# Kernel optimization log

Measured on AMD Instinct MI355X. Metric: run time of the kernel, lower is better.

## Reference

```python
import jax, jax.numpy as jnp
import numpy as np

N, E = 50000, 800000
F_IN, C1, H1 = 128, 16, 4        # conv1: 128 -> 16 per head, 4 heads (concat -> 64)
F_MID = C1 * H1                   # 64
N_CLASSES, H2 = 10, 1             # conv2: 64 -> 10, 1 head, no concat
NEG_SLOPE = 0.2


def setup_inputs() -> dict:
    key = jax.random.key(0)
    ks = jax.random.split(key, 12)
    s1 = 1.0 / np.sqrt(F_IN)
    s2 = 1.0 / np.sqrt(F_MID)
    return {
        "x": jax.random.normal(ks[0], (N, F_IN), dtype=jnp.float32),
        "edge_index": jax.random.randint(ks[1], (2, E), 0, N, dtype=jnp.int64),
        # conv1 params (GATv2: separate lin_l / lin_r, per-head attention vector, bias)
        "W1l": jax.random.normal(ks[2], (F_IN, H1 * C1), dtype=jnp.float32) * s1,
        "W1r": jax.random.normal(ks[3], (F_IN, H1 * C1), dtype=jnp.float32) * s1,
        "att1": jax.random.normal(ks[4], (H1, C1), dtype=jnp.float32) * s1,
        "b1": jnp.zeros((H1 * C1,), dtype=jnp.float32),
        # conv2 params
        "W2l": jax.random.normal(ks[5], (F_MID, H2 * N_CLASSES), dtype=jnp.float32) * s2,
        "W2r": jax.random.normal(ks[6], (F_MID, H2 * N_CLASSES), dtype=jnp.float32) * s2,
        "att2": jax.random.normal(ks[7], (H2, N_CLASSES), dtype=jnp.float32) * s2,
        "b2": jnp.zeros((N_CLASSES,), dtype=jnp.float32),
    }


def gatv2_conv(x, Wl, Wr, att, b, src, dst, concat):
    """GATv2Conv (add_self_loops=False, eval mode). src -> dst message passing."""
    H, C = att.shape
    n = x.shape[0]
    xl = (x @ Wl).reshape(n, H, C)   # source-side transform (also the value)
    xr = (x @ Wr).reshape(n, H, C)   # target-side transform
    # per-edge GATv2 score: att . LeakyReLU(xl[src] + xr[dst])
    e = jax.nn.leaky_relu(xl[src] + xr[dst], NEG_SLOPE)          # [E, H, C]
    logits = jnp.einsum("ehc,hc->eh", e, att)                    # [E, H]
    # segment softmax over incoming edges of each dst node
    m = jax.ops.segment_max(logits, dst, num_segments=n)         # [N, H]
    ex = jnp.exp(logits - m[dst])
    denom = jax.ops.segment_sum(ex, dst, num_segments=n)         # [N, H]
    alpha = ex / denom[dst]                                      # [E, H]
    out = jax.ops.segment_sum(alpha[:, :, None] * xl[src], dst, num_segments=n)  # [N, H, C]
    out = out.reshape(n, H * C) if concat else out.mean(axis=1)
    return out + b


def reference(x, edge_index, W1l, W1r, att1, b1, W2l, W2r, att2, b2):
    src, dst = edge_index[0], edge_index[1]
    h = jax.nn.elu(gatv2_conv(x, W1l, W1r, att1, b1, src, dst, concat=True))
    return gatv2_conv(h, W2l, W2r, att2, b2, src, dst, concat=False)
```

## Files before the change

kernel.cpp:

```cpp
#include <hip/hip_runtime.h>
#include <math.h>

#define NN 50000
#define NE 800000
#define FIN 128
#define NC 10
#define NEG 0.2f

#define NB 196
#define CHUNK 4096
#define P1B ((NE + CHUNK - 1) / CHUNK)
#define CAP 5120
#define G1T ((NN + 127) / 128)

typedef unsigned int uint;
typedef unsigned char uchar;
typedef _Float16 h2 __attribute__((ext_vector_type(2)));
typedef __fp16 hb2 __attribute__((ext_vector_type(2)));
union U2H { uint u; h2 h; };

__device__ __forceinline__ uint pkrtz_u(float a, float b) {
    union { hb2 f; uint u; } r;
    r.f = __builtin_amdgcn_cvt_pkrtz(a, b);
    return r.u;
}

__device__ __forceinline__ float dot2f(h2 a, h2 b, float c) {
#if __has_builtin(__builtin_amdgcn_fdot2)
    return __builtin_amdgcn_fdot2(a, b, c, false);
#else
    return fmaf((float)a.x, (float)b.x, fmaf((float)a.y, (float)b.y, c));
#endif
}

__device__ __forceinline__ h2 lrelu2(h2 v) {
    return __builtin_elementwise_max(v, v * (_Float16)0.2f);
}

template<int CTRL>
__device__ __forceinline__ float dpp_add(float x) {
    int y = __builtin_amdgcn_update_dpp(0, __float_as_int(x), CTRL, 0xF, 0xF, true);
    return x + __int_as_float(y);
}
__device__ __forceinline__ float red8(float t) {
    t = dpp_add<0xB1>(t);
    t = dpp_add<0x4E>(t);
    t = dpp_add<0x141>(t);
    return t;
}

__device__ __forceinline__ int excl_scan256(int v, int* sc) {
    const int t = threadIdx.x;
    sc[t] = v;
    __syncthreads();
    for (int o = 1; o < 256; o <<= 1) {
        int u = (t >= o) ? sc[t - o] : 0;
        __syncthreads();
        sc[t] += u;
        __syncthreads();
    }
    return sc[t] - v;
}


__global__ void k_zinit(int* __restrict__ g) {
    if (threadIdx.x < NB) g[threadIdx.x] = 0;
}


__device__ void pass1_body(const int* __restrict__ ei, uint* __restrict__ temp,
                           int* __restrict__ gcursor, char* smraw) {
    uint*  pk = (uint*)smraw;
    uchar* bk = (uchar*)(smraw + 16384);
    int* h  = (int*)(smraw + 20480);
    int* h2_ = (int*)(smraw + 21504);
    int* gb = (int*)(smraw + 22528);
    int* lb = (int*)(smraw + 23552);
    int* sc = (int*)(smraw + 24576);
    const int t = threadIdx.x;
    const int e0 = blockIdx.x * CHUNK;
    const int cnt = min(CHUNK, NE - e0);

    h[t] = 0; h2_[t] = 0;
    __syncthreads();
    for (int i = t; i < cnt; i += 256) {
        int d = ei[NE + e0 + i];
        atomicAdd(&h[d >> 8], 1);
    }
    __syncthreads();
    const int hv = h[t];
    const int ex = excl_scan256(hv, sc);
    lb[t] = ex;
    if (t < NB && hv > 0) gb[t] = atomicAdd(&gcursor[t], hv);
    __syncthreads();
    for (int i = t; i < cnt; i += 256) {
        int s = ei[e0 + i];
        int d = ei[NE + e0 + i];
        int b = d >> 8;
        int r = atomicAdd(&h2_[b], 1);
        int pos = lb[b] + r;
        pk[pos] = ((uint)s << 8) | ((uint)d & 255u);
        bk[pos] = (uchar)b;
    }
    __syncthreads();
    for (int i = t; i < cnt; i += 256) {
        uint v = pk[i];
        int b = bk[i];
        int pos = gb[b] + (i - lb[b]);
        if (pos < CAP) temp[b * CAP + pos] = v;
    }
}

__device__ void gemm1_body(const float* __restrict__ x, const float* __restrict__ W,
                           uint* __restrict__ oh2, int n0, char* smraw) {
    uint (*Wsh)[64]  = (uint(*)[64])smraw;
    uint (*xTh)[128] = (uint(*)[128])(smraw + 16384);
    const int t = threadIdx.x;

    for (int i = t; i < 4096; i += 256) {
        int kp = i >> 6, col = i & 63;
        Wsh[kp][col] = pkrtz_u(W[(2 * kp) * 64 + col], W[(2 * kp + 1) * 64 + col]);
    }

    const int tn = t >> 4;
    const int tc = t & 15;
    float acc[8][4] = {};
    const int sn = t >> 1;
    const int kp0 = (t & 1) * 8;

    for (int kc = 0; kc < FIN; kc += 32) {
        __syncthreads();
        {
            int gn = n0 + sn;
            float4 v0, v1, v2, v3;
            if (gn < NN) {
                const float4* xr_ = (const float4*)(x + (size_t)gn * FIN + kc + kp0 * 2);
                v0 = xr_[0]; v1 = xr_[1]; v2 = xr_[2]; v3 = xr_[3];
            } else {
                v0 = v1 = v2 = v3 = make_float4(0.f, 0.f, 0.f, 0.f);
            }
            xTh[kp0 + 0][sn] = pkrtz_u(v0.x, v0.y);
            xTh[kp0 + 1][sn] = pkrtz_u(v0.z, v0.w);
            xTh[kp0 + 2][sn] = pkrtz_u(v1.x, v1.y);
            xTh[kp0 + 3][sn] = pkrtz_u(v1.z, v1.w);
            xTh[kp0 + 4][sn] = pkrtz_u(v2.x, v2.y);
            xTh[kp0 + 5][sn] = pkrtz_u(v2.z, v2.w);
            xTh[kp0 + 6][sn] = pkrtz_u(v3.x, v3.y);
            xTh[kp0 + 7][sn] = pkrtz_u(v3.z, v3.w);
        }
        __syncthreads();
        const int kpc = kc >> 1;
#pragma unroll
        for (int kp = 0; kp < 16; ++kp) {
            uint4 wv = *(const uint4*)&Wsh[kpc + kp][tc * 4];
            uint4 xa = *(const uint4*)&xTh[kp][tn * 8];
            uint4 xb = *(const uint4*)&xTh[kp][tn * 8 + 4];
            U2H w0, w1, w2, w3, x0, x1, x2, x3, x4, x5, x6, x7;
            w0.u = wv.x; w1.u = wv.y; w2.u = wv.z; w3.u = wv.w;
            x0.u = xa.x; x1.u = xa.y; x2.u = xa.z; x3.u = xa.w;
            x4.u = xb.x; x5.u = xb.y; x6.u = xb.z; x7.u = xb.w;
            h2 xs[8] = {x0.h, x1.h, x2.h, x3.h, x4.h, x5.h, x6.h, x7.h};
#pragma unroll
            for (int i = 0; i < 8; ++i) {
                acc[i][0] = dot2f(xs[i], w0.h, acc[i][0]);
                acc[i][1] = dot2f(xs[i], w1.h, acc[i][1]);
                acc[i][2] = dot2f(xs[i], w2.h, acc[i][2]);
                acc[i][3] = dot2f(xs[i], w3.h, acc[i][3]);
            }
        }
    }
#pragma unroll
    for (int i = 0; i < 8; ++i) {
        int n = n0 + tn * 8 + i;
        if (n < NN) {
            uint p0 = pkrtz_u(acc[i][0], acc[i][1]);
            uint p1 = pkrtz_u(acc[i][2], acc[i][3]);
            *(uint2*)&oh2[(size_t)n * 32 + tc * 2] = make_uint2(p0, p1);
        }
    }
}

__global__ __launch_bounds__(256) void k_fusedA(const float* __restrict__ x,
                                                const int* __restrict__ ei,
                                                const float* __restrict__ W1l,
                                                const float* __restrict__ W1r,
                                                uint* __restrict__ xlh2,
                                                uint* __restrict__ xrh2,
                                                uint* __restrict__ temp,
                                                int* __restrict__ gcursor) {
    __shared__ __align__(16) char smraw[25600];
    if (blockIdx.x < P1B) {
        pass1_body(ei, temp, gcursor, smraw);
    } else {
        int g = blockIdx.x - P1B;
        bool left = g < G1T;
        int n0 = (left ? g : g - G1T) * 128;
        gemm1_body(x, left ? W1l : W1r, left ? xlh2 : xrh2, n0, smraw);
    }
}


__global__ __launch_bounds__(256) void k_pass2(const uint* __restrict__ temp,
                                               const int* __restrict__ gcursor,
                                               int* __restrict__ rowptr,
                                               int* __restrict__ deg,
                                               int* __restrict__ csr_src) {
    __shared__ uint P[CAP];
    __shared__ int nh[256], nbx[256], ncur[256], sc[256];
    __shared__ int csrbase_s;
    const int t = threadIdx.x;
    const int b = blockIdx.x;

    int gc = (t < NB) ? gcursor[t] : 0;
    int base_ex = excl_scan256(gc, sc);
    if (t == b) csrbase_s = base_ex;
    nh[t] = 0; ncur[t] = 0;
    __syncthreads();
    const int csrbase = csrbase_s;
    const int cnt = min(gcursor[b], CAP);

    for (int i = t; i < cnt; i += 256) {
        uint v = temp[b * CAP + i];
        P[i] = v;
        atomicAdd(&nh[v & 255u], 1);
    }
    __syncthreads();
    const int c = nh[t];
    const int nb_ex = excl_scan256(c, sc);
    nbx[t] = nb_ex;
    const int gnode = b * 256 + t;
    if (gnode < NN) { rowptr[gnode] = csrbase + nb_ex; deg[gnode] = c; }
    __syncthreads();
    for (int i = t; i < cnt; i += 256) {
        uint v = P[i];
        int l = (int)(v & 255u);
        int r = atomicAdd(&ncur[l], 1);
        csr_src[csrbase + nbx[l] + r] = (int)(v >> 8);
    }
}


__global__ __launch_bounds__(256) void k_agg1(const uint* __restrict__ xlh2,
                                              const uint* __restrict__ xrh2,
                                              const int* __restrict__ rowptr,
                                              const int* __restrict__ deg,
                                              const int* __restrict__ csr_src,
                                              const float* __restrict__ att1,
                                              const float* __restrict__ b1,
                                              uint* __restrict__ hbh2) {
    const int node = blockIdx.x * 4 + (threadIdx.x >> 6);
    if (node >= NN) return;
    const int lane = threadIdx.x & 63;
    const int fl = lane & 31;
    const int hid = lane >> 5;
    float2 av = *(const float2*)&att1[2 * fl];
    U2H att; att.u = pkrtz_u(av.x, av.y);
    U2H xrf; xrf.u = xrh2[(size_t)node * 32 + fl];
    const int start = rowptr[node];
    const int dg = deg[node];
    const int permbase = (lane & 32) >> 3;

    float denom = 0.f, acc0 = 0.f, acc1 = 0.f;
    for (int base = 0; base < dg; base += 64) {
        int idx = base + lane;
        int srcs = (idx < dg) ? csr_src[start + idx] : 0;
        int rem = dg - base; if (rem > 64) rem = 64;
        int iters = (rem + 1) >> 1;
        int thr = (rem - hid + 1) >> 1;
        for (int jj = 0; jj < iters; jj += 8) {
            int s[8]; U2H v[8];
#pragma unroll
            for (int k = 0; k < 8; ++k)
                s[k] = __builtin_amdgcn_ds_bpermute((jj + k) * 8 + permbase, srcs);
#pragma unroll
            for (int k = 0; k < 8; ++k)
                v[k].u = xlh2[(size_t)s[k] * 32 + fl];
#pragma unroll
            for (int k = 0; k < 8; ++k) {
                float tl = red8(dot2f(lrelu2(v[k].h + xrf.h), att.h, 0.f));
                float e = (jj + k < thr) ? __expf(tl) : 0.f;
                denom += e;
                acc0 = fmaf(e, (float)v[k].h.x, acc0);
                acc1 = fmaf(e, (float)v[k].h.y, acc1);
            }
        }
    }
    denom += __shfl_xor(denom, 32);
    acc0  += __shfl_xor(acc0, 32);
    acc1  += __shfl_xor(acc1, 32);
    if (lane < 32) {
        float r = (dg > 0) ? (1.0f / denom) : 0.f;
        float2 bv = *(const float2*)&b1[2 * fl];
        float o0 = fmaf(acc0, r, bv.x);
        float o1 = fmaf(acc1, r, bv.y);
        o0 = o0 > 0.f ? o0 : expm1f(o0);
        o1 = o1 > 0.f ? o1 : expm1f(o1);
        hbh2[(size_t)node * 32 + fl] = pkrtz_u(o0, o1);
    }
}


__global__ __launch_bounds__(256) void k_gemm2(const uint* __restrict__ hbh2,
                                               const float* __restrict__ W2l,
                                               const float* __restrict__ W2r,
                                               uint* __restrict__ xl2h,
                                               uint* __restrict__ xr2h) {
    int n = blockIdx.x * 256 + threadIdx.x;
    if (n >= NN) return;
    float al[NC] = {}, ar[NC] = {};
    const uint4* hr4 = (const uint4*)(hbh2 + (size_t)n * 32);
#pragma unroll
    for (int q = 0; q < 8; ++q) {
        uint4 qq = hr4[q];
        uint uu[4] = {qq.x, qq.y, qq.z, qq.w};
#pragma unroll
        for (int j = 0; j < 4; ++j) {
            U2H hh; hh.u = uu[j];
            float f0 = (float)hh.h.x, f1 = (float)hh.h.y;
            int k = q * 8 + j * 2;
            const float* wl0 = W2l + k * NC;
            const float* wr0 = W2r + k * NC;
#pragma unroll
            for (int c = 0; c < NC; ++c) {
                al[c] = fmaf(f0, wl0[c], fmaf(f1, wl0[NC + c], al[c]));
                ar[c] = fmaf(f0, wr0[c], fmaf(f1, wr0[NC + c], ar[c]));
            }
        }
    }
    uint p0 = pkrtz_u(al[0], al[1]);
    uint p1 = pkrtz_u(al[2], al[3]);
    uint p2 = pkrtz_u(al[4], al[5]);
    uint p3 = pkrtz_u(al[6], al[7]);
    uint p4 = pkrtz_u(al[8], al[9]);
    *(uint4*)&xl2h[(size_t)n * 8]     = make_uint4(p0, p1, p2, p3);
    *(uint4*)&xl2h[(size_t)n * 8 + 4] = make_uint4(p4, 0u, 0u, 0u);
    p0 = pkrtz_u(ar[0], ar[1]);
    p1 = pkrtz_u(ar[2], ar[3]);
    p2 = pkrtz_u(ar[4], ar[5]);
    p3 = pkrtz_u(ar[6], ar[7]);
    p4 = pkrtz_u(ar[8], ar[9]);
    *(uint4*)&xr2h[(size_t)n * 8]     = make_uint4(p0, p1, p2, p3);
    *(uint4*)&xr2h[(size_t)n * 8 + 4] = make_uint4(p4, 0u, 0u, 0u);
}


__global__ __launch_bounds__(256) void k_agg2(const uint* __restrict__ xl2h,
                                              const uint* __restrict__ xr2h,
                                              const int* __restrict__ rowptr,
                                              const int* __restrict__ deg,
                                              const int* __restrict__ csr_src,
                                              const float* __restrict__ att2,
                                              const float* __restrict__ b2,
                                              float* __restrict__ out) {
    const int node = blockIdx.x * 4 + (threadIdx.x >> 6);
    if (node >= NN) return;
    const int lane = threadIdx.x & 63;
    const int fp = lane & 7;
    const int eg = lane >> 3;
    U2H att;
    if (fp < 5) {
        float2 av = *(const float2*)&att2[2 * fp];
        att.u = pkrtz_u(av.x, av.y);
    } else {
        att.u = 0;
    }
    U2H xrf; xrf.u = xr2h[(size_t)node * 8 + fp];
    const int start = rowptr[node];
    const int dg = deg[node];
    const int permbase = eg * 4;

    float denom = 0.f, acc0 = 0.f, acc1 = 0.f;
    for (int base = 0; base < dg; base += 64) {
        int idx = base + lane;
        int srcs = (idx < dg) ? csr_src[start + idx] : 0;
        int rem = dg - base; if (rem > 64) rem = 64;
        int iters = (rem + 7) >> 3;
        int thr = (rem - eg + 7) >> 3;
        for (int jj = 0; jj < iters; jj += 4) {
            int s[4]; U2H v[4];
#pragma unroll
            for (int k = 0; k < 4; ++k)
                s[k] = __builtin_amdgcn_ds_bpermute((jj + k) * 32 + permbase, srcs);
#pragma unroll
            for (int k = 0; k < 4; ++k)
                v[k].u = xl2h[(size_t)s[k] * 8 + fp];
#pragma unroll
            for (int k = 0; k < 4; ++k) {
                float tl = red8(dot2f(lrelu2(v[k].h + xrf.h), att.h, 0.f));
                float e = (jj + k < thr) ? __expf(tl) : 0.f;
                denom += e;
                acc0 = fmaf(e, (float)v[k].h.x, acc0);
                acc1 = fmaf(e, (float)v[k].h.y, acc1);
            }
        }
    }
#pragma unroll
    for (int m = 8; m <= 32; m <<= 1) {
        denom += __shfl_xor(denom, m);
        acc0  += __shfl_xor(acc0, m);
        acc1  += __shfl_xor(acc1, m);
    }
    if (lane < 5) {
        float r = (dg > 0) ? (1.0f / denom) : 0.f;
        float2 o;
        o.x = fmaf(acc0, r, b2[2 * fp]);
        o.y = fmaf(acc1, r, b2[2 * fp + 1]);
        *(float2*)&out[(size_t)node * NC + 2 * fp] = o;
    }
}


extern "C" void kernel_launch(void* const* d_in, const int* in_sizes, int n_in,
                              void* d_out, int out_size, void* d_ws, size_t ws_size,
                              hipStream_t stream) {
    const float* x    = (const float*)d_in[0];
    const int*   ei   = (const int*)d_in[1];
    const float* W1l  = (const float*)d_in[2];
    const float* W1r  = (const float*)d_in[3];
    const float* att1 = (const float*)d_in[4];
    const float* b1   = (const float*)d_in[5];
    const float* W2l  = (const float*)d_in[6];
    const float* W2r  = (const float*)d_in[7];
    const float* att2 = (const float*)d_in[8];
    const float* b2   = (const float*)d_in[9];
    float* out = (float*)d_out;

    char* w = (char*)d_ws;
    size_t off = 0;
    auto alloc = [&](size_t bytes) -> void* {
        void* p = w + off;
        off = (off + bytes + 255) & ~(size_t)255;
        return p;
    };
    uint* xlh2   = (uint*)alloc((size_t)NN * 32 * 4);
    uint* xrh2   = (uint*)alloc((size_t)NN * 32 * 4);
    uint* hbh2   = (uint*)alloc((size_t)NN * 32 * 4);
    uint* xl2h   = (uint*)alloc((size_t)NN * 8 * 4);
    uint* xr2h   = (uint*)alloc((size_t)NN * 8 * 4);
    uint* temp   = (uint*)alloc((size_t)NB * CAP * 4);
    int*  gcursor = (int*)alloc((size_t)NB * 4);
    int*  rowptr  = (int*)alloc((size_t)NN * 4);
    int*  deg     = (int*)alloc((size_t)NN * 4);
    int*  csr_src = (int*)alloc((size_t)NE * 4);

    k_zinit<<<1, 256, 0, stream>>>(gcursor);
    k_fusedA<<<P1B + 2 * G1T, 256, 0, stream>>>(x, ei, W1l, W1r, xlh2, xrh2, temp, gcursor);
    k_pass2<<<NB, 256, 0, stream>>>(temp, gcursor, rowptr, deg, csr_src);
    k_agg1<<<(NN + 3) / 4, 256, 0, stream>>>(xlh2, xrh2, rowptr, deg, csr_src, att1, b1, hbh2);
    k_gemm2<<<(NN + 255) / 256, 256, 0, stream>>>(hbh2, W2l, W2r, xl2h, xr2h);
    k_agg2<<<(NN + 3) / 4, 256, 0, stream>>>(xl2h, xr2h, rowptr, deg, csr_src, att2, b2, out);
}
```

Baseline: 110.8 us.

## Replace global-atomic bucket scatter with per-chunk offsets matrix; persistent agg1 loop

Pass1 now writes each chunk's locally bucket-sorted edges contiguously and records per-bucket offsets in a matrix, replacing global atomic cursors. Pass2 gathers its bucket's segments from every chunk via a scan over that matrix. This removes the zero-init kernel and the global atomics. Agg1 becomes a grid-stride persistent kernel that reads source indices directly from the CSR with padding instead of using bpermute. The cost is a serial per-thread copy loop in pass2 (one thread per chunk) and some wasted loads on the padded edges.

```diff
diff --git a/kernel.cpp b/kernel.cpp
--- a/kernel.cpp
+++ b/kernel.cpp
@@ -12,6 +12,8 @@
 #define P1B ((NE + CHUNK - 1) / CHUNK)
 #define CAP 5120
 #define G1T ((NN + 127) / 128)
+#define LBW 200
+#define A1B 2048
 
 typedef unsigned int uint;
 typedef unsigned char uchar;
@@ -63,22 +65,15 @@
 }
 
 
-__global__ void k_zinit(int* __restrict__ g) {
-    if (threadIdx.x < NB) g[threadIdx.x] = 0;
-}
-
-
 __device__ void pass1_body(const int* __restrict__ ei, uint* __restrict__ temp,
-                           int* __restrict__ gcursor, char* smraw) {
-    uint*  pk = (uint*)smraw;
-    uchar* bk = (uchar*)(smraw + 16384);
-    int* h  = (int*)(smraw + 20480);
-    int* h2_ = (int*)(smraw + 21504);
-    int* gb = (int*)(smraw + 22528);
-    int* lb = (int*)(smraw + 23552);
-    int* sc = (int*)(smraw + 24576);
+                           int* __restrict__ lbmat, char* smraw) {
+    uint* pk = (uint*)smraw;
+    int* h   = (int*)(smraw + 16384);
+    int* h2_ = (int*)(smraw + 17408);
+    int* sc  = (int*)(smraw + 18432);
     const int t = threadIdx.x;
-    const int e0 = blockIdx.x * CHUNK;
+    const int B = blockIdx.x;
+    const int e0 = B * CHUNK;
     const int cnt = min(CHUNK, NE - e0);
 
     h[t] = 0; h2_[t] = 0;
@@ -90,25 +85,19 @@
     __syncthreads();
     const int hv = h[t];
     const int ex = excl_scan256(hv, sc);
-    lb[t] = ex;
-    if (t < NB && hv > 0) gb[t] = atomicAdd(&gcursor[t], hv);
+    if (t < NB) lbmat[B * LBW + t] = ex;
+    if (t == NB - 1) lbmat[B * LBW + NB] = ex + hv;
+    h2_[t] = ex;
     __syncthreads();
     for (int i = t; i < cnt; i += 256) {
         int s = ei[e0 + i];
         int d = ei[NE + e0 + i];
         int b = d >> 8;
-        int r = atomicAdd(&h2_[b], 1);
-        int pos = lb[b] + r;
+        int pos = atomicAdd(&h2_[b], 1);
         pk[pos] = ((uint)s << 8) | ((uint)d & 255u);
-        bk[pos] = (uchar)b;
-    }
-    __syncthreads();
-    for (int i = t; i < cnt; i += 256) {
-        uint v = pk[i];
-        int b = bk[i];
-        int pos = gb[b] + (i - lb[b]);
-        if (pos < CAP) temp[b * CAP + pos] = v;
-    }
+    }
+    __syncthreads();
+    for (int i = t; i < cnt; i += 256) temp[B * CHUNK + i] = pk[i];
 }
 
 __device__ void gemm1_body(const float* __restrict__ x, const float* __restrict__ W,
@@ -187,10 +176,10 @@
                                                 uint* __restrict__ xlh2,
                                                 uint* __restrict__ xrh2,
                                                 uint* __restrict__ temp,
-                                                int* __restrict__ gcursor) {
+                                                int* __restrict__ lbmat) {
     __shared__ __align__(16) char smraw[25600];
     if (blockIdx.x < P1B) {
-        pass1_body(ei, temp, gcursor, smraw);
+        pass1_body(ei, temp, lbmat, smraw);
     } else {
         int g = blockIdx.x - P1B;
         bool left = g < G1T;
@@ -201,29 +190,36 @@
 
 
 __global__ __launch_bounds__(256) void k_pass2(const uint* __restrict__ temp,
-                                               const int* __restrict__ gcursor,
+                                               const int* __restrict__ lbmat,
                                                int* __restrict__ rowptr,
                                                int* __restrict__ deg,
                                                int* __restrict__ csr_src) {
     __shared__ uint P[CAP];
     __shared__ int nh[256], nbx[256], ncur[256], sc[256];
-    __shared__ int csrbase_s;
     const int t = threadIdx.x;
     const int b = blockIdx.x;
 
-    int gc = (t < NB) ? gcursor[t] : 0;
-    int base_ex = excl_scan256(gc, sc);
-    if (t == b) csrbase_s = base_ex;
+    int lbv = 0, len = 0;
+    if (t < P1B) {
+        lbv = lbmat[t * LBW + b];
+        len = lbmat[t * LBW + b + 1] - lbv;
+    }
+    const int colstart = excl_scan256(len, sc);
+    __syncthreads();
+    const int cnt = sc[255];
+    __syncthreads();
+    (void)excl_scan256(lbv, sc);
+    __syncthreads();
+    const int csrbase = sc[255];
+    __syncthreads();
     nh[t] = 0; ncur[t] = 0;
     __syncthreads();
-    const int csrbase = csrbase_s;
-    const int cnt = min(gcursor[b], CAP);
-
-    for (int i = t; i < cnt; i += 256) {
-        uint v = temp[b * CAP + i];
-        P[i] = v;
-        atomicAdd(&nh[v & 255u], 1);
-    }
+    if (t < P1B) {
+        const uint* src = temp + t * CHUNK + lbv;
+        for (int i = 0; i < len; ++i) P[colstart + i] = src[i];
+    }
+    __syncthreads();
+    for (int i = t; i < cnt; i += 256) atomicAdd(&nh[P[i] & 255u], 1);
     __syncthreads();
     const int c = nh[t];
     const int nb_ex = excl_scan256(c, sc);
@@ -237,6 +233,7 @@
         int r = atomicAdd(&ncur[l], 1);
         csr_src[csrbase + nbx[l] + r] = (int)(v >> 8);
     }
+    if (b == 0 && t < 64) csr_src[NE + t] = 0;
 }
 
 
@@ -248,54 +245,52 @@
                                               const float* __restrict__ att1,
                                               const float* __restrict__ b1,
                                               uint* __restrict__ hbh2) {
-    const int node = blockIdx.x * 4 + (threadIdx.x >> 6);
-    if (node >= NN) return;
     const int lane = threadIdx.x & 63;
     const int fl = lane & 31;
     const int hid = lane >> 5;
     float2 av = *(const float2*)&att1[2 * fl];
     U2H att; att.u = pkrtz_u(av.x, av.y);
-    U2H xrf; xrf.u = xrh2[(size_t)node * 32 + fl];
-    const int start = rowptr[node];
-    const int dg = deg[node];
-    const int permbase = (lane & 32) >> 3;
-
-    float denom = 0.f, acc0 = 0.f, acc1 = 0.f;
-    for (int base = 0; base < dg; base += 64) {
-        int idx = base + lane;
-        int srcs = (idx < dg) ? csr_src[start + idx] : 0;
-        int rem = dg - base; if (rem > 64) rem = 64;
-        int iters = (rem + 1) >> 1;
-        int thr = (rem - hid + 1) >> 1;
-        for (int jj = 0; jj < iters; jj += 8) {
-            int s[8]; U2H v[8];
-#pragma unroll
-            for (int k = 0; k < 8; ++k)
-                s[k] = __builtin_amdgcn_ds_bpermute((jj + k) * 8 + permbase, srcs);
-#pragma unroll
-            for (int k = 0; k < 8; ++k)
-                v[k].u = xlh2[(size_t)s[k] * 32 + fl];
-#pragma unroll
-            for (int k = 0; k < 8; ++k) {
+    float2 bv = *(const float2*)&b1[2 * fl];
+    const int wave0 = __builtin_amdgcn_readfirstlane(blockIdx.x * 4 + (threadIdx.x >> 6));
+
+    for (int node = wave0; node < NN; node += A1B * 4) {
+        U2H xrf; xrf.u = xrh2[(size_t)node * 32 + fl];
+        const int start = rowptr[node];
+        const int dg = deg[node];
+        const int* sp = csr_src + start;
+
+        float denom = 0.f, acc0 = 0.f, acc1 = 0.f;
+        const int niter = (dg + 1) >> 1;
+        for (int jj = 0; jj < niter; jj += 4) {
+            int e8[8];
+#pragma unroll
+            for (int k = 0; k < 8; ++k) e8[k] = sp[2 * jj + k];
+            U2H v[4];
+#pragma unroll
+            for (int k = 0; k < 4; ++k) {
+                int src = hid ? e8[2 * k + 1] : e8[2 * k];
+                v[k].u = xlh2[(size_t)src * 32 + fl];
+            }
+#pragma unroll
+            for (int k = 0; k < 4; ++k) {
                 float tl = red8(dot2f(lrelu2(v[k].h + xrf.h), att.h, 0.f));
-                float e = (jj + k < thr) ? __expf(tl) : 0.f;
+                float e = (2 * (jj + k) + hid < dg) ? __expf(tl) : 0.f;
                 denom += e;
                 acc0 = fmaf(e, (float)v[k].h.x, acc0);
                 acc1 = fmaf(e, (float)v[k].h.y, acc1);
             }
         }
-    }
-    denom += __shfl_xor(denom, 32);
-    acc0  += __shfl_xor(acc0, 32);
-    acc1  += __shfl_xor(acc1, 32);
-    if (lane < 32) {
-        float r = (dg > 0) ? (1.0f / denom) : 0.f;
-        float2 bv = *(const float2*)&b1[2 * fl];
-        float o0 = fmaf(acc0, r, bv.x);
-        float o1 = fmaf(acc1, r, bv.y);
-        o0 = o0 > 0.f ? o0 : expm1f(o0);
-        o1 = o1 > 0.f ? o1 : expm1f(o1);
-        hbh2[(size_t)node * 32 + fl] = pkrtz_u(o0, o1);
+        denom += __shfl_xor(denom, 32);
+        acc0  += __shfl_xor(acc0, 32);
+        acc1  += __shfl_xor(acc1, 32);
+        if (lane < 32) {
+            float r = (dg > 0) ? (1.0f / denom) : 0.f;
+            float o0 = fmaf(acc0, r, bv.x);
+            float o1 = fmaf(acc1, r, bv.y);
+            o0 = o0 > 0.f ? o0 : expm1f(o0);
+            o1 = o1 > 0.f ? o1 : expm1f(o1);
+            hbh2[(size_t)node * 32 + fl] = pkrtz_u(o0, o1);
+        }
     }
 }
 
@@ -437,16 +432,15 @@
     uint* hbh2   = (uint*)alloc((size_t)NN * 32 * 4);
     uint* xl2h   = (uint*)alloc((size_t)NN * 8 * 4);
     uint* xr2h   = (uint*)alloc((size_t)NN * 8 * 4);
-    uint* temp   = (uint*)alloc((size_t)NB * CAP * 4);
-    int*  gcursor = (int*)alloc((size_t)NB * 4);
-    int*  rowptr  = (int*)alloc((size_t)NN * 4);
-    int*  deg     = (int*)alloc((size_t)NN * 4);
-    int*  csr_src = (int*)alloc((size_t)NE * 4);
-
-    k_zinit<<<1, 256, 0, stream>>>(gcursor);
-    k_fusedA<<<P1B + 2 * G1T, 256, 0, stream>>>(x, ei, W1l, W1r, xlh2, xrh2, temp, gcursor);
-    k_pass2<<<NB, 256, 0, stream>>>(temp, gcursor, rowptr, deg, csr_src);
-    k_agg1<<<(NN + 3) / 4, 256, 0, stream>>>(xlh2, xrh2, rowptr, deg, csr_src, att1, b1, hbh2);
+    uint* temp   = (uint*)alloc((size_t)P1B * CHUNK * 4);
+    int*  lbmat  = (int*)alloc((size_t)P1B * LBW * 4);
+    int*  rowptr = (int*)alloc((size_t)NN * 4);
+    int*  deg    = (int*)alloc((size_t)NN * 4);
+    int*  csr_src = (int*)alloc((size_t)(NE + 64) * 4);
+
+    k_fusedA<<<P1B + 2 * G1T, 256, 0, stream>>>(x, ei, W1l, W1r, xlh2, xrh2, temp, lbmat);
+    k_pass2<<<NB, 256, 0, stream>>>(temp, lbmat, rowptr, deg, csr_src);
+    k_agg1<<<A1B, 256, 0, stream>>>(xlh2, xrh2, rowptr, deg, csr_src, att1, b1, hbh2);
     k_gemm2<<<(NN + 255) / 256, 256, 0, stream>>>(hbh2, W2l, W2r, xl2h, xr2h);
     k_agg2<<<(NN + 3) / 4, 256, 0, stream>>>(xl2h, xr2h, rowptr, deg, csr_src, att2, b2, out);
 }
```

Result: slower. 121.8 us (+9.9%).
